# Performance work log

Hardware: AMD Instinct MI355X
Metric: run time of the kernel (lower is better)

## Reference

```python
import jax, jax.numpy as jnp
import numpy as np

KS = 7            # kernel_size
CH = 3            # channels
THRESH = 128      # threshold (0-255 scale)
TOL = 0.2         # tolerance
PAD = KS // 2


def setup_inputs() -> dict:
    key = jax.random.key(0)
    x = jax.random.uniform(key, (16, CH, 1024, 1024), dtype=jnp.float32)
    return {"x": x}


def reference(x):
    # 1) threshold -> binary map
    cond = (x >= THRESH / 255.0).astype(x.dtype)            # [B,C,H,W]
    # 2) reflect pad spatial dims by k//2
    padded = jnp.pad(cond, ((0, 0), (0, 0), (PAD, PAD), (PAD, PAD)), mode='reflect')
    # 3) depthwise box-sum conv (all-ones kernel, groups=C)
    kernel = jnp.ones((CH, 1, KS, KS), dtype=x.dtype)        # OIHW, I=1 per group
    csum = jax.lax.conv_general_dilated(
        padded, kernel,
        window_strides=(1, 1), padding='VALID',
        feature_group_count=CH,
        dimension_numbers=('NCHW', 'OIHW', 'NCHW'))          # [B,C,H,W]
    # 4) tolerance band mask (note: integer floor-div first, matching torch)
    half = KS * KS // 2
    lo = half * TOL
    hi = half * (1.0 - TOL)
    mask = ((csum >= lo) & (csum <= hi)).astype(x.dtype)
    # 5) zero out masked pixels
    return x * (1.0 - mask)
```

## Files before the change

kernel.cpp:

```cpp
#include <hip/hip_runtime.h>


constexpr int H = 1024;
constexpr int W = 1024;
constexpr int BH = 8;
constexpr int NBANDS = H / BH;
constexpr int STEPS = BH + 6;

__global__ __launch_bounds__(256)
void backedge_kernel(const float* __restrict__ x, float* __restrict__ out) {
    const int lane = threadIdx.x & 63;
    const int wv   = threadIdx.x >> 6;
    const int band = blockIdx.x * 4 + wv;
    const int n    = blockIdx.y;
    const int r0   = band * BH;
    const float* __restrict__ xi = x   + (size_t)n * (size_t)(H * W);
    float*       __restrict__ oi = out + (size_t)n * (size_t)(H * W);
    const int off = 4 * lane;
    const float THR = 128.0f / 255.0f;

    unsigned int hring[7][4];
#pragma unroll
    for (int i = 0; i < 7; ++i)
#pragma unroll
        for (int q = 0; q < 4; ++q) hring[i][q] = 0u;
    unsigned int vs[4] = {0u, 0u, 0u, 0u};

#pragma unroll
    for (int s = 0; s < STEPS; ++s) {
        int g = r0 - 3 + s;
        g = (g < 0) ? -g : g;
        g = (g >= H) ? (2 * H - 2 - g) : g;
        const float* rp = xi + (size_t)g * W;
        float4 a[4];
#pragma unroll
        for (int q = 0; q < 4; ++q)
            a[q] = *(const float4*)(rp + q * 256 + off);

        unsigned int m = 0;
#pragma unroll
        for (int q = 0; q < 4; ++q) {
            m |= ((unsigned)(a[q].x >= THR)) << (4 * q + 0);
            m |= ((unsigned)(a[q].y >= THR)) << (4 * q + 1);
            m |= ((unsigned)(a[q].z >= THR)) << (4 * q + 2);
            m |= ((unsigned)(a[q].w >= THR)) << (4 * q + 3);
        }

        const unsigned int up = __shfl_up(m, 1);
        const unsigned int dn = __shfl_down(m, 1);
        const unsigned int hi = __shfl(m, 63);
        const unsigned int lo = __shfl(m, 0);
        const unsigned int SL = (lane == 0) ? (hi << 4) : up;
        const unsigned int SR = (lane == 63) ? (lo >> 4) : dn;

        unsigned int hp[4];
#pragma unroll
        for (int q = 0; q < 4; ++q) {
            unsigned int w = ((SL >> (4 * q + 1)) & 7u)
                           | (((m >> (4 * q)) & 0xFu) << 3)
                           | (((SR >> (4 * q)) & 7u) << 7);
            if (q == 0 && lane == 0) {
                w |= ((m >> 3) & 1u) | (((m >> 2) & 1u) << 1)
                   | (((m >> 1) & 1u) << 2);
            }
            if (q == 3 && lane == 63) {
                w |= (((m >> 14) & 1u) << 7) | (((m >> 13) & 1u) << 8)
                   | (((m >> 12) & 1u) << 9);
            }
            const unsigned int h0 = __popc((w >> 0) & 0x7Fu);
            const unsigned int h1 = __popc((w >> 1) & 0x7Fu);
            const unsigned int h2 = __popc((w >> 2) & 0x7Fu);
            const unsigned int h3 = __popc((w >> 3) & 0x7Fu);
            hp[q] = h0 | (h1 << 8) | (h2 << 16) | (h3 << 24);
        }

#pragma unroll
        for (int q = 0; q < 4; ++q) vs[q] += hp[q] - hring[0][q];
#pragma unroll
        for (int i = 0; i < 6; ++i)
#pragma unroll
            for (int q = 0; q < 4; ++q) hring[i][q] = hring[i + 1][q];
#pragma unroll
        for (int q = 0; q < 4; ++q) hring[6][q] = hp[q];

        if (s >= 6) {
            const int orow = r0 + s - 6;
            const float* xp = xi + (size_t)orow * W;
            float*       op = oi + (size_t)orow * W;
#pragma unroll
            for (int q = 0; q < 4; ++q) {
                const float4 b = *(const float4*)(xp + q * 256 + off);
                const unsigned int v = vs[q];
                float4 o;
                o.x = ((((v      ) & 0xFFu) - 5u) <= 14u) ? 0.0f : b.x;
                o.y = ((((v >>  8) & 0xFFu) - 5u) <= 14u) ? 0.0f : b.y;
                o.z = ((((v >> 16) & 0xFFu) - 5u) <= 14u) ? 0.0f : b.z;
                o.w = ((((v >> 24)        ) - 5u) <= 14u) ? 0.0f : b.w;
                *(float4*)(op + q * 256 + off) = o;
            }
        }
    }
}

extern "C" void kernel_launch(void* const* d_in, const int* in_sizes, int n_in,
                              void* d_out, int out_size, void* d_ws, size_t ws_size,
                              hipStream_t stream) {
    const float* x = (const float*)d_in[0];
    float* out = (float*)d_out;
    (void)in_sizes; (void)n_in; (void)d_ws; (void)ws_size; (void)out_size;
    dim3 grid(NBANDS / 4, 16 * 3);
    backedge_kernel<<<grid, dim3(256), 0, stream>>>(x, out);
}
```

Before: 362.9 us.

## Keep input rows in register ring, prefetch next row, nontemporal stores, larger bands

Each output row now takes its x values from a 5-deep register ring of loaded rows instead of reloading them from global memory, and the next row is prefetched one step ahead. The horizontal-sum history is packed into nibbles to save registers, band height doubles to cut halo overhead, stores become nontemporal, and launch bounds request 3 blocks per CU. In exchange the kernel uses more registers, and the grid has half as many blocks.

```diff
diff --git a/kernel.cpp b/kernel.cpp
--- a/kernel.cpp
+++ b/kernel.cpp
@@ -3,11 +3,29 @@
 
 constexpr int H = 1024;
 constexpr int W = 1024;
-constexpr int BH = 8;
+constexpr int BH = 16;
 constexpr int NBANDS = H / BH;
 constexpr int STEPS = BH + 6;
+constexpr int D = 5;
 
-__global__ __launch_bounds__(256)
+typedef float vfloat4 __attribute__((ext_vector_type(4)));
+
+__device__ __forceinline__ void nt_store4(float* p, float4 v) {
+    vfloat4 t;
+    t.x = v.x; t.y = v.y; t.z = v.z; t.w = v.w;
+    __builtin_nontemporal_store(t, (vfloat4*)p);
+}
+
+__device__ __forceinline__ unsigned expand4(unsigned n) {
+    unsigned t = (n | (n << 8)) & 0x00FF00FFu;
+    return (t | (t << 4)) & 0x0F0F0F0Fu;
+}
+__device__ __forceinline__ unsigned compress4(unsigned b) {
+    unsigned t = (b | (b >> 4)) & 0x00FF00FFu;
+    return (t | (t >> 8)) & 0x0000FFFFu;
+}
+
+__global__ __launch_bounds__(256, 3)
 void backedge_kernel(const float* __restrict__ x, float* __restrict__ out) {
     const int lane = threadIdx.x & 63;
     const int wv   = threadIdx.x >> 6;
@@ -19,31 +37,41 @@
     const int off = 4 * lane;
     const float THR = 128.0f / 255.0f;
 
-    unsigned int hring[7][4];
+    float4 ring[D][4];
+    unsigned int hn[7][2];
 #pragma unroll
-    for (int i = 0; i < 7; ++i)
+    for (int i = 0; i < 7; ++i) { hn[i][0] = 0u; hn[i][1] = 0u; }
+    unsigned int vs[4] = {0u, 0u, 0u, 0u};
+
+    {
+        int g = r0 - 3;
+        g = (g < 0) ? -g : g;
+        const float* rp = xi + (size_t)g * W;
 #pragma unroll
-        for (int q = 0; q < 4; ++q) hring[i][q] = 0u;
-    unsigned int vs[4] = {0u, 0u, 0u, 0u};
+        for (int q = 0; q < 4; ++q)
+            ring[0][q] = *(const float4*)(rp + q * 256 + off);
+    }
 
 #pragma unroll
     for (int s = 0; s < STEPS; ++s) {
-        int g = r0 - 3 + s;
-        g = (g < 0) ? -g : g;
-        g = (g >= H) ? (2 * H - 2 - g) : g;
-        const float* rp = xi + (size_t)g * W;
-        float4 a[4];
+        if (s + 1 < STEPS) {
+            int g = r0 - 3 + (s + 1);
+            g = (g < 0) ? -g : g;
+            g = (g >= H) ? (2 * H - 2 - g) : g;
+            const float* rp = xi + (size_t)g * W;
 #pragma unroll
-        for (int q = 0; q < 4; ++q)
-            a[q] = *(const float4*)(rp + q * 256 + off);
+            for (int q = 0; q < 4; ++q)
+                ring[(s + 1) % D][q] = *(const float4*)(rp + q * 256 + off);
+        }
 
         unsigned int m = 0;
 #pragma unroll
         for (int q = 0; q < 4; ++q) {
-            m |= ((unsigned)(a[q].x >= THR)) << (4 * q + 0);
-            m |= ((unsigned)(a[q].y >= THR)) << (4 * q + 1);
-            m |= ((unsigned)(a[q].z >= THR)) << (4 * q + 2);
-            m |= ((unsigned)(a[q].w >= THR)) << (4 * q + 3);
+            const float4 aq = ring[s % D][q];
+            m |= ((unsigned)(aq.x >= THR)) << (4 * q + 0);
+            m |= ((unsigned)(aq.y >= THR)) << (4 * q + 1);
+            m |= ((unsigned)(aq.z >= THR)) << (4 * q + 2);
+            m |= ((unsigned)(aq.w >= THR)) << (4 * q + 3);
         }
 
         const unsigned int up = __shfl_up(m, 1);
@@ -74,29 +102,31 @@
             hp[q] = h0 | (h1 << 8) | (h2 << 16) | (h3 << 24);
         }
 
+        vs[0] += hp[0] - expand4(hn[0][0] & 0xFFFFu);
+        vs[1] += hp[1] - expand4(hn[0][0] >> 16);
+        vs[2] += hp[2] - expand4(hn[0][1] & 0xFFFFu);
+        vs[3] += hp[3] - expand4(hn[0][1] >> 16);
 #pragma unroll
-        for (int q = 0; q < 4; ++q) vs[q] += hp[q] - hring[0][q];
-#pragma unroll
-        for (int i = 0; i < 6; ++i)
-#pragma unroll
-            for (int q = 0; q < 4; ++q) hring[i][q] = hring[i + 1][q];
-#pragma unroll
-        for (int q = 0; q < 4; ++q) hring[6][q] = hp[q];
+        for (int i = 0; i < 6; ++i) {
+            hn[i][0] = hn[i + 1][0];
+            hn[i][1] = hn[i + 1][1];
+        }
+        hn[6][0] = compress4(hp[0]) | (compress4(hp[1]) << 16);
+        hn[6][1] = compress4(hp[2]) | (compress4(hp[3]) << 16);
 
         if (s >= 6) {
             const int orow = r0 + s - 6;
-            const float* xp = xi + (size_t)orow * W;
-            float*       op = oi + (size_t)orow * W;
+            float* op = oi + (size_t)orow * W;
 #pragma unroll
             for (int q = 0; q < 4; ++q) {
-                const float4 b = *(const float4*)(xp + q * 256 + off);
+                const float4 b = ring[(s - 3) % D][q];
                 const unsigned int v = vs[q];
                 float4 o;
                 o.x = ((((v      ) & 0xFFu) - 5u) <= 14u) ? 0.0f : b.x;
                 o.y = ((((v >>  8) & 0xFFu) - 5u) <= 14u) ? 0.0f : b.y;
                 o.z = ((((v >> 16) & 0xFFu) - 5u) <= 14u) ? 0.0f : b.z;
                 o.w = ((((v >> 24)        ) - 5u) <= 14u) ? 0.0f : b.w;
-                *(float4*)(op + q * 256 + off) = o;
+                nt_store4(op + q * 256 + off, o);
             }
         }
     }
```

After: 352.4 us. 2.9% less time.
